# Kernel optimization log

Hardware: AMD Instinct MI355X
Metric: run time of the kernel (lower is better)

## Reference

```python
import jax, jax.numpy as jnp
import numpy as np

DIM = 1024
NUM_HEADS = 16
WINDOW_SIZE = 512
HEAD_DIM = DIM // NUM_HEADS
SCALE = HEAD_DIM ** (-0.5)


def setup_inputs() -> dict:
    key = jax.random.key(0)
    kq, kk, kv = jax.random.split(key, 3)
    shape = (2, NUM_HEADS, 2048, HEAD_DIM)
    q = jax.random.normal(kq, shape, dtype=jnp.float32)
    k = jax.random.normal(kk, shape, dtype=jnp.float32)
    v = jax.random.normal(kv, shape, dtype=jnp.float32)
    return {"q": q, "k": k, "v": v}


def reference(q, k, v):
    B, H, N, D = q.shape
    pos = jnp.arange(N)
    # causal + sliding window: col <= row and col >= row - w + 1
    window_mask = (pos[None, :] <= pos[:, None]) & (pos[None, :] >= pos[:, None] - WINDOW_SIZE + 1)  # (N, N)
    attn = jnp.einsum("bhnd,bhmd->bhnm", q, k) * SCALE  # (B, H, N, N)
    attn = jnp.where(window_mask[None, None], attn, -jnp.inf)
    attn = jax.nn.softmax(attn, axis=-1)
    attn = jnp.nan_to_num(attn, nan=0.0)
    return jnp.einsum("bhnm,bhmd->bhnd", attn, v)
```

## Files before the change

### kernel.cpp

```cpp
#include <hip/hip_runtime.h>


#define SEQ 2048
#define HD  64

typedef short short8 __attribute__((ext_vector_type(8)));
typedef float f32x4  __attribute__((ext_vector_type(4)));
typedef int   i32x4  __attribute__((ext_vector_type(4)));

static __device__ inline unsigned short f2bf(float f){
  union{float f; unsigned u;} un; un.f=f;
  return (unsigned short)((un.u + 0x7FFFu + ((un.u>>16)&1u))>>16);
}
static __device__ inline int swz(int row){ return (row&3)|(((row>>3)&1)<<2); }

__global__ __launch_bounds__(512) void swa_fused(
    const float* __restrict__ q, const float* __restrict__ k,
    const float* __restrict__ v, float* __restrict__ out)
{
  __shared__ unsigned short Ks[2][4096];
  __shared__ unsigned short Vsh[2][4096];

  const int tid=threadIdx.x, bid=blockIdx.x;
  const int mt=bid&15, bh=bid>>4, m0=mt*128;
  const long base=(long)bh*SEQ*HD;
  const int wv=tid>>6, lane=tid&63, quad=lane>>4, l16=lane&15;
  const int qrow=m0+wv*16+l16;
  const int h=wv>>2;

  short8 qa[2];
  {
    const float C=0.18033688011112042f;
    const float* qp=q+base+(long)qrow*HD+quad*8;
    #pragma unroll
    for(int kk=0;kk<2;++kk){
      float4 f0=*(const float4*)(qp+kk*32);
      float4 f1=*(const float4*)(qp+kk*32+4);
      short8 a;
      a[0]=(short)f2bf(f0.x*C); a[1]=(short)f2bf(f0.y*C);
      a[2]=(short)f2bf(f0.z*C); a[3]=(short)f2bf(f0.w*C);
      a[4]=(short)f2bf(f1.x*C); a[5]=(short)f2bf(f1.y*C);
      a[6]=(short)f2bf(f1.z*C); a[7]=(short)f2bf(f1.w*C);
      qa[kk]=a;
    }
  }

  const int rbase=8*(l16>>2)+(l16&3);
  const int swk=(l16&3)|(((l16>>2)&1)<<2);
  const int swv=(l16&3)|(((l16>>3)&1)<<2);
  int kaoff[2][4], vboff[2][4];
  #pragma unroll
  for(int kk=0;kk<2;++kk){
    #pragma unroll
    for(int nt=0;nt<4;++nt)
      kaoff[kk][nt]=(rbase+(nt&1)*4+(nt>>1)*32)*64+(((quad+4*kk)^swk)*8);
    #pragma unroll
    for(int dt=0;dt<4;++dt)
      vboff[kk][dt]=(dt*16+l16)*64+(((quad+4*kk)^swv)*8);
  }

  const int kr=tid>>3, klc=tid&7;
  const int kwaddr=kr*64+((klc^swz(kr))*8);
  const int vw=tid>>6, vd=tid&63;
  const int vwaddr=vd*64+((vw^swz(vd))*8);
  const float* kg=k+base;
  const float* vg=v+base;

  f32x4 oacc[4];
  #pragma unroll
  for(int dt=0;dt<4;++dt) oacc[dt]=(f32x4){0.f,0.f,0.f,0.f};
  float lrun=0.f;

  const int Tb =2*mt+1;
  const int Tlo=(2*mt>8)?(2*mt-8):0;
  const int myTb=2*mt+h;
  const bool clip=(myTb>=8);
  const int myTlo=clip?(myTb-8):0;

  {
    const float* kt=kg+(long)Tlo*4096;
    const float* vt=vg+(long)Tlo*4096;
    float4 kf0=*(const float4*)(kt+kr*64+klc*8);
    float4 kf1=*(const float4*)(kt+kr*64+klc*8+4);
    float vf[8];
    #pragma unroll
    for(int j=0;j<8;++j) vf[j]=vt[(vw*8+j)*64+vd];
    unsigned short hk[8];
    hk[0]=f2bf(kf0.x); hk[1]=f2bf(kf0.y); hk[2]=f2bf(kf0.z); hk[3]=f2bf(kf0.w);
    hk[4]=f2bf(kf1.x); hk[5]=f2bf(kf1.y); hk[6]=f2bf(kf1.z); hk[7]=f2bf(kf1.w);
    *(uint4*)&Ks[0][kwaddr]=*(uint4*)hk;
    unsigned short hv[8];
    #pragma unroll
    for(int j=0;j<8;++j) hv[j]=f2bf(vf[j]);
    *(uint4*)&Vsh[0][vwaddr]=*(uint4*)hv;
  }
  __syncthreads();

  for(int t=Tlo;t<=Tb;++t){
    const int buf=(t-Tlo)&1;
    const bool pf=(t<Tb);

    float4 kf0,kf1; float vf[8];
    if(pf){
      const float* kt=kg+(long)(t+1)*4096;
      const float* vt=vg+(long)(t+1)*4096;
      kf0=*(const float4*)(kt+kr*64+klc*8);
      kf1=*(const float4*)(kt+kr*64+klc*8+4);
      #pragma unroll
      for(int j=0;j<8;++j) vf[j]=vt[(vw*8+j)*64+vd];
    }

    if(t>=myTlo && t<=myTb){
      f32x4 sacc[4];
      #pragma unroll
      for(int nt=0;nt<4;++nt) sacc[nt]=(f32x4){0.f,0.f,0.f,0.f};
      #pragma unroll
      for(int kk=0;kk<2;++kk)
        #pragma unroll
        for(int nt=0;nt<4;++nt){
          short8 ka=*(const short8*)&Ks[buf][kaoff[kk][nt]];
          sacc[nt]=__builtin_amdgcn_mfma_f32_16x16x32_bf16(ka,qa[kk],sacc[nt],0,0,0);
        }

      unsigned pp[8];
      float ls=0.f;
      const bool msk=(t==myTb)||(clip&&t==myTlo);
      #pragma unroll
      for(int nt=0;nt<4;++nt){
        float e0=__builtin_amdgcn_exp2f(sacc[nt][0]);
        float e1=__builtin_amdgcn_exp2f(sacc[nt][1]);
        float e2=__builtin_amdgcn_exp2f(sacc[nt][2]);
        float e3=__builtin_amdgcn_exp2f(sacc[nt][3]);
        if(msk){
          const int kb0=t*64+8*quad+(nt&1)*4+(nt>>1)*32;
          e0=((kb0+0<=qrow)&&(kb0+0+511>=qrow))?e0:0.f;
          e1=((kb0+1<=qrow)&&(kb0+1+511>=qrow))?e1:0.f;
          e2=((kb0+2<=qrow)&&(kb0+2+511>=qrow))?e2:0.f;
          e3=((kb0+3<=qrow)&&(kb0+3+511>=qrow))?e3:0.f;
        }
        ls+=e0+e1+e2+e3;
        pp[nt*2+0]=(__float_as_uint(e1)&0xFFFF0000u)|(__float_as_uint(e0)>>16);
        pp[nt*2+1]=(__float_as_uint(e3)&0xFFFF0000u)|(__float_as_uint(e2)>>16);
      }
      lrun+=ls;
      i32x4 i0={(int)pp[0],(int)pp[1],(int)pp[2],(int)pp[3]};
      i32x4 i1={(int)pp[4],(int)pp[5],(int)pp[6],(int)pp[7]};
      short8 pa0=*(short8*)&i0;
      short8 pa1=*(short8*)&i1;

      #pragma unroll
      for(int dt=0;dt<4;++dt){
        short8 vb0=*(const short8*)&Vsh[buf][vboff[0][dt]];
        short8 vb1=*(const short8*)&Vsh[buf][vboff[1][dt]];
        oacc[dt]=__builtin_amdgcn_mfma_f32_16x16x32_bf16(pa0,vb0,oacc[dt],0,0,0);
        oacc[dt]=__builtin_amdgcn_mfma_f32_16x16x32_bf16(pa1,vb1,oacc[dt],0,0,0);
      }
    }

    if(pf){
      unsigned short hk[8];
      hk[0]=f2bf(kf0.x); hk[1]=f2bf(kf0.y); hk[2]=f2bf(kf0.z); hk[3]=f2bf(kf0.w);
      hk[4]=f2bf(kf1.x); hk[5]=f2bf(kf1.y); hk[6]=f2bf(kf1.z); hk[7]=f2bf(kf1.w);
      *(uint4*)&Ks[buf^1][kwaddr]=*(uint4*)hk;
      unsigned short hv[8];
      #pragma unroll
      for(int j=0;j<8;++j) hv[j]=f2bf(vf[j]);
      *(uint4*)&Vsh[buf^1][vwaddr]=*(uint4*)hv;
    }
    __syncthreads();
  }

  lrun+=__shfl_xor(lrun,16);
  lrun+=__shfl_xor(lrun,32);
  float linv=1.0f/lrun;
  #pragma unroll
  for(int r=0;r<4;++r){
    float lr=__shfl(linv,quad*4+r);
    const int orow=m0+wv*16+quad*4+r;
    #pragma unroll
    for(int dt=0;dt<4;++dt)
      out[base+(long)orow*HD+dt*16+l16]=oacc[dt][r]*lr;
  }
}

extern "C" void kernel_launch(void* const* d_in, const int* in_sizes, int n_in,
                              void* d_out, int out_size, void* d_ws, size_t ws_size,
                              hipStream_t stream) {
  (void)in_sizes; (void)n_in; (void)out_size; (void)d_ws; (void)ws_size;
  const float* q=(const float*)d_in[0];
  const float* k=(const float*)d_in[1];
  const float* v=(const float*)d_in[2];
  float* o=(float*)d_out;
  hipLaunchKernelGGL(swa_fused, dim3(512), dim3(512), 0, stream, q, k, v, o);
}
```

Measured before the change: 108.4 us.

## Pre-convert K/V to swizzled bf16 images and stream them via global_load_lds

Adds a prep kernel that converts K and V from fp32 to bf16 once, writing them to workspace already in the swizzled (and transposed, for V) shared-memory layout. The attention kernel then copies each tile straight into LDS with 16-byte global_load_lds, replacing the per-block fp32 loads, conversions and LDS stores. This removes the redundant conversion work repeated across the overlapping windows and halves the bytes read per tile. In exchange it adds a second launch and a workspace round trip, and the async LDS loads rely on the existing barrier for ordering.

```diff
diff --git a/kernel.cpp b/kernel.cpp
--- a/kernel.cpp
+++ b/kernel.cpp
@@ -14,9 +14,44 @@
 }
 static __device__ inline int swz(int row){ return (row&3)|(((row>>3)&1)<<2); }
 
+static __device__ __forceinline__ void gload16(const void* g, void* l){
+  __builtin_amdgcn_global_load_lds(
+      (const __attribute__((address_space(1))) void*)g,
+      (__attribute__((address_space(3))) void*)l,
+      16, 0, 0);
+}
+
+__global__ __launch_bounds__(512) void swa_prep(
+    const float* __restrict__ k, const float* __restrict__ v,
+    unsigned short* __restrict__ kp, unsigned short* __restrict__ vp)
+{
+  const int tid=threadIdx.x, bid=blockIdx.x;
+  const long fbase=(long)bid*4096;
+  const long ib  =(long)bid*4096;
+
+  {
+    const int kr=tid>>3, klc=tid&7;
+    const float* kt=k+fbase+kr*64+klc*8;
+    float4 f0=*(const float4*)kt;
+    float4 f1=*(const float4*)(kt+4);
+    unsigned short h[8];
+    h[0]=f2bf(f0.x); h[1]=f2bf(f0.y); h[2]=f2bf(f0.z); h[3]=f2bf(f0.w);
+    h[4]=f2bf(f1.x); h[5]=f2bf(f1.y); h[6]=f2bf(f1.z); h[7]=f2bf(f1.w);
+    *(uint4*)&kp[ib + kr*64 + ((klc^swz(kr))*8)] = *(uint4*)h;
+  }
+  {
+    const int vw=tid>>6, vd=tid&63;
+    const float* vt=v+fbase;
+    unsigned short h[8];
+    #pragma unroll
+    for(int j=0;j<8;++j) h[j]=f2bf(vt[(vw*8+j)*64+vd]);
+    *(uint4*)&vp[ib + vd*64 + ((vw^swz(vd))*8)] = *(uint4*)h;
+  }
+}
+
 __global__ __launch_bounds__(512) void swa_fused(
-    const float* __restrict__ q, const float* __restrict__ k,
-    const float* __restrict__ v, float* __restrict__ out)
+    const float* __restrict__ q, const unsigned short* __restrict__ kp,
+    const unsigned short* __restrict__ vp, float* __restrict__ out)
 {
   __shared__ unsigned short Ks[2][4096];
   __shared__ unsigned short Vsh[2][4096];
@@ -59,12 +94,10 @@
       vboff[kk][dt]=(dt*16+l16)*64+(((quad+4*kk)^swv)*8);
   }
 
-  const int kr=tid>>3, klc=tid&7;
-  const int kwaddr=kr*64+((klc^swz(kr))*8);
-  const int vw=tid>>6, vd=tid&63;
-  const int vwaddr=vd*64+((vw^swz(vd))*8);
-  const float* kg=k+base;
-  const float* vg=v+base;
+  const unsigned short* kimg = kp + (long)bh*32*4096 + tid*8;
+  const unsigned short* vimg = vp + (long)bh*32*4096 + tid*8;
+  unsigned short* kdst = &Ks[0][wv*512];
+  unsigned short* vdst = &Vsh[0][wv*512];
 
   f32x4 oacc[4];
   #pragma unroll
@@ -77,37 +110,16 @@
   const bool clip=(myTb>=8);
   const int myTlo=clip?(myTb-8):0;
 
-  {
-    const float* kt=kg+(long)Tlo*4096;
-    const float* vt=vg+(long)Tlo*4096;
-    float4 kf0=*(const float4*)(kt+kr*64+klc*8);
-    float4 kf1=*(const float4*)(kt+kr*64+klc*8+4);
-    float vf[8];
-    #pragma unroll
-    for(int j=0;j<8;++j) vf[j]=vt[(vw*8+j)*64+vd];
-    unsigned short hk[8];
-    hk[0]=f2bf(kf0.x); hk[1]=f2bf(kf0.y); hk[2]=f2bf(kf0.z); hk[3]=f2bf(kf0.w);
-    hk[4]=f2bf(kf1.x); hk[5]=f2bf(kf1.y); hk[6]=f2bf(kf1.z); hk[7]=f2bf(kf1.w);
-    *(uint4*)&Ks[0][kwaddr]=*(uint4*)hk;
-    unsigned short hv[8];
-    #pragma unroll
-    for(int j=0;j<8;++j) hv[j]=f2bf(vf[j]);
-    *(uint4*)&Vsh[0][vwaddr]=*(uint4*)hv;
-  }
+  gload16(kimg+(long)Tlo*4096, kdst);
+  gload16(vimg+(long)Tlo*4096, vdst);
   __syncthreads();
 
   for(int t=Tlo;t<=Tb;++t){
     const int buf=(t-Tlo)&1;
-    const bool pf=(t<Tb);
-
-    float4 kf0,kf1; float vf[8];
-    if(pf){
-      const float* kt=kg+(long)(t+1)*4096;
-      const float* vt=vg+(long)(t+1)*4096;
-      kf0=*(const float4*)(kt+kr*64+klc*8);
-      kf1=*(const float4*)(kt+kr*64+klc*8+4);
-      #pragma unroll
-      for(int j=0;j<8;++j) vf[j]=vt[(vw*8+j)*64+vd];
+
+    if(t<Tb){
+      gload16(kimg+(long)(t+1)*4096, kdst+(buf^1)*4096);
+      gload16(vimg+(long)(t+1)*4096, vdst+(buf^1)*4096);
     }
 
     if(t>=myTlo && t<=myTb){
@@ -157,16 +169,6 @@
       }
     }
 
-    if(pf){
-      unsigned short hk[8];
-      hk[0]=f2bf(kf0.x); hk[1]=f2bf(kf0.y); hk[2]=f2bf(kf0.z); hk[3]=f2bf(kf0.w);
-      hk[4]=f2bf(kf1.x); hk[5]=f2bf(kf1.y); hk[6]=f2bf(kf1.z); hk[7]=f2bf(kf1.w);
-      *(uint4*)&Ks[buf^1][kwaddr]=*(uint4*)hk;
-      unsigned short hv[8];
-      #pragma unroll
-      for(int j=0;j<8;++j) hv[j]=f2bf(vf[j]);
-      *(uint4*)&Vsh[buf^1][vwaddr]=*(uint4*)hv;
-    }
     __syncthreads();
   }
 
@@ -186,10 +188,13 @@
 extern "C" void kernel_launch(void* const* d_in, const int* in_sizes, int n_in,
                               void* d_out, int out_size, void* d_ws, size_t ws_size,
                               hipStream_t stream) {
-  (void)in_sizes; (void)n_in; (void)out_size; (void)d_ws; (void)ws_size;
+  (void)in_sizes; (void)n_in; (void)out_size; (void)ws_size;
   const float* q=(const float*)d_in[0];
   const float* k=(const float*)d_in[1];
   const float* v=(const float*)d_in[2];
   float* o=(float*)d_out;
-  hipLaunchKernelGGL(swa_fused, dim3(512), dim3(512), 0, stream, q, k, v, o);
-}
+  unsigned short* kp=(unsigned short*)d_ws;
+  unsigned short* vp=kp + (long)32*32*4096;
+  hipLaunchKernelGGL(swa_prep,  dim3(1024), dim3(512), 0, stream, k, v, kp, vp);
+  hipLaunchKernelGGL(swa_fused, dim3(512),  dim3(512), 0, stream, q, kp, vp, o);
+}
```

After: 109.9 us. About the same (+1.4%).

## Process two K/V tiles per pipeline stage to halve block barriers

Applied to the files above, without the earlier changes.

Restructures the double-buffered loop so each iteration loads, converts and consumes two 64-row K/V tiles instead of one. This halves the number of __syncthreads and makes each prefetch twice as deep. It also adds a min-blocks hint of 4 to launch_bounds. The cost is twice the LDS (64KB per block) and more prefetch registers, which could limit occupancy or cause spills under the tighter register budget.

```diff
diff --git a/kernel.cpp b/kernel.cpp
--- a/kernel.cpp
+++ b/kernel.cpp
@@ -14,12 +14,12 @@
 }
 static __device__ inline int swz(int row){ return (row&3)|(((row>>3)&1)<<2); }
 
-__global__ __launch_bounds__(512) void swa_fused(
+__global__ __launch_bounds__(512,4) void swa_fused(
     const float* __restrict__ q, const float* __restrict__ k,
     const float* __restrict__ v, float* __restrict__ out)
 {
-  __shared__ unsigned short Ks[2][4096];
-  __shared__ unsigned short Vsh[2][4096];
+  __shared__ unsigned short Ks[2][2][4096];
+  __shared__ unsigned short Vsh[2][2][4096];
 
   const int tid=threadIdx.x, bid=blockIdx.x;
   const int mt=bid&15, bh=bid>>4, m0=mt*128;
@@ -76,96 +76,106 @@
   const int myTb=2*mt+h;
   const bool clip=(myTb>=8);
   const int myTlo=clip?(myTb-8):0;
-
-  {
-    const float* kt=kg+(long)Tlo*4096;
-    const float* vt=vg+(long)Tlo*4096;
-    float4 kf0=*(const float4*)(kt+kr*64+klc*8);
-    float4 kf1=*(const float4*)(kt+kr*64+klc*8+4);
-    float vf[8];
-    #pragma unroll
-    for(int j=0;j<8;++j) vf[j]=vt[(vw*8+j)*64+vd];
+  const int nR=(Tb-Tlo+2)>>1;
+
+  #pragma unroll
+  for(int s=0;s<2;++s){
+    const float* kt=kg+(long)(Tlo+s)*4096;
+    const float* vt=vg+(long)(Tlo+s)*4096;
+    float4 f0=*(const float4*)(kt+kr*64+klc*8);
+    float4 f1=*(const float4*)(kt+kr*64+klc*8+4);
     unsigned short hk[8];
-    hk[0]=f2bf(kf0.x); hk[1]=f2bf(kf0.y); hk[2]=f2bf(kf0.z); hk[3]=f2bf(kf0.w);
-    hk[4]=f2bf(kf1.x); hk[5]=f2bf(kf1.y); hk[6]=f2bf(kf1.z); hk[7]=f2bf(kf1.w);
-    *(uint4*)&Ks[0][kwaddr]=*(uint4*)hk;
+    hk[0]=f2bf(f0.x); hk[1]=f2bf(f0.y); hk[2]=f2bf(f0.z); hk[3]=f2bf(f0.w);
+    hk[4]=f2bf(f1.x); hk[5]=f2bf(f1.y); hk[6]=f2bf(f1.z); hk[7]=f2bf(f1.w);
+    *(uint4*)&Ks[0][s][kwaddr]=*(uint4*)hk;
     unsigned short hv[8];
     #pragma unroll
-    for(int j=0;j<8;++j) hv[j]=f2bf(vf[j]);
-    *(uint4*)&Vsh[0][vwaddr]=*(uint4*)hv;
+    for(int j=0;j<8;++j) hv[j]=f2bf(vt[(vw*8+j)*64+vd]);
+    *(uint4*)&Vsh[0][s][vwaddr]=*(uint4*)hv;
   }
   __syncthreads();
 
-  for(int t=Tlo;t<=Tb;++t){
-    const int buf=(t-Tlo)&1;
-    const bool pf=(t<Tb);
-
-    float4 kf0,kf1; float vf[8];
+  for(int r=0;r<nR;++r){
+    const int buf=r&1;
+    const bool pf=(r+1<nR);
+
+    float4 kf0[2],kf1[2]; float vf[2][8];
     if(pf){
-      const float* kt=kg+(long)(t+1)*4096;
-      const float* vt=vg+(long)(t+1)*4096;
-      kf0=*(const float4*)(kt+kr*64+klc*8);
-      kf1=*(const float4*)(kt+kr*64+klc*8+4);
       #pragma unroll
-      for(int j=0;j<8;++j) vf[j]=vt[(vw*8+j)*64+vd];
-    }
-
-    if(t>=myTlo && t<=myTb){
-      f32x4 sacc[4];
+      for(int s=0;s<2;++s){
+        const int tn=Tlo+2*r+2+s;
+        const float* kt=kg+(long)tn*4096;
+        const float* vt=vg+(long)tn*4096;
+        kf0[s]=*(const float4*)(kt+kr*64+klc*8);
+        kf1[s]=*(const float4*)(kt+kr*64+klc*8+4);
+        #pragma unroll
+        for(int j=0;j<8;++j) vf[s][j]=vt[(vw*8+j)*64+vd];
+      }
+    }
+
+    #pragma unroll
+    for(int s=0;s<2;++s){
+      const int t=Tlo+2*r+s;
+      if(t>=myTlo && t<=myTb){
+        f32x4 sacc[4];
+        #pragma unroll
+        for(int nt=0;nt<4;++nt) sacc[nt]=(f32x4){0.f,0.f,0.f,0.f};
+        #pragma unroll
+        for(int kk=0;kk<2;++kk)
+          #pragma unroll
+          for(int nt=0;nt<4;++nt){
+            short8 ka=*(const short8*)&Ks[buf][s][kaoff[kk][nt]];
+            sacc[nt]=__builtin_amdgcn_mfma_f32_16x16x32_bf16(ka,qa[kk],sacc[nt],0,0,0);
+          }
+
+        unsigned pp[8];
+        float ls=0.f;
+        const bool msk=(t==myTb)||(clip&&t==myTlo);
+        #pragma unroll
+        for(int nt=0;nt<4;++nt){
+          float e0=__builtin_amdgcn_exp2f(sacc[nt][0]);
+          float e1=__builtin_amdgcn_exp2f(sacc[nt][1]);
+          float e2=__builtin_amdgcn_exp2f(sacc[nt][2]);
+          float e3=__builtin_amdgcn_exp2f(sacc[nt][3]);
+          if(msk){
+            const int kb0=t*64+8*quad+(nt&1)*4+(nt>>1)*32;
+            e0=((kb0+0<=qrow)&&(kb0+0+511>=qrow))?e0:0.f;
+            e1=((kb0+1<=qrow)&&(kb0+1+511>=qrow))?e1:0.f;
+            e2=((kb0+2<=qrow)&&(kb0+2+511>=qrow))?e2:0.f;
+            e3=((kb0+3<=qrow)&&(kb0+3+511>=qrow))?e3:0.f;
+          }
+          ls+=e0+e1+e2+e3;
+          pp[nt*2+0]=(__float_as_uint(e1)&0xFFFF0000u)|(__float_as_uint(e0)>>16);
+          pp[nt*2+1]=(__float_as_uint(e3)&0xFFFF0000u)|(__float_as_uint(e2)>>16);
+        }
+        lrun+=ls;
+        i32x4 i0={(int)pp[0],(int)pp[1],(int)pp[2],(int)pp[3]};
+        i32x4 i1={(int)pp[4],(int)pp[5],(int)pp[6],(int)pp[7]};
+        short8 pa0=*(short8*)&i0;
+        short8 pa1=*(short8*)&i1;
+
+        #pragma unroll
+        for(int dt=0;dt<4;++dt){
+          short8 vb0=*(const short8*)&Vsh[buf][s][vboff[0][dt]];
+          short8 vb1=*(const short8*)&Vsh[buf][s][vboff[1][dt]];
+          oacc[dt]=__builtin_amdgcn_mfma_f32_16x16x32_bf16(pa0,vb0,oacc[dt],0,0,0);
+          oacc[dt]=__builtin_amdgcn_mfma_f32_16x16x32_bf16(pa1,vb1,oacc[dt],0,0,0);
+        }
+      }
+    }
+
+    if(pf){
       #pragma unroll
-      for(int nt=0;nt<4;++nt) sacc[nt]=(f32x4){0.f,0.f,0.f,0.f};
-      #pragma unroll
-      for(int kk=0;kk<2;++kk)
-        #pragma unroll
-        for(int nt=0;nt<4;++nt){
-          short8 ka=*(const short8*)&Ks[buf][kaoff[kk][nt]];
-          sacc[nt]=__builtin_amdgcn_mfma_f32_16x16x32_bf16(ka,qa[kk],sacc[nt],0,0,0);
-        }
-
-      unsigned pp[8];
-      float ls=0.f;
-      const bool msk=(t==myTb)||(clip&&t==myTlo);
-      #pragma unroll
-      for(int nt=0;nt<4;++nt){
-        float e0=__builtin_amdgcn_exp2f(sacc[nt][0]);
-        float e1=__builtin_amdgcn_exp2f(sacc[nt][1]);
-        float e2=__builtin_amdgcn_exp2f(sacc[nt][2]);
-        float e3=__builtin_amdgcn_exp2f(sacc[nt][3]);
-        if(msk){
-          const int kb0=t*64+8*quad+(nt&1)*4+(nt>>1)*32;
-          e0=((kb0+0<=qrow)&&(kb0+0+511>=qrow))?e0:0.f;
-          e1=((kb0+1<=qrow)&&(kb0+1+511>=qrow))?e1:0.f;
-          e2=((kb0+2<=qrow)&&(kb0+2+511>=qrow))?e2:0.f;
-          e3=((kb0+3<=qrow)&&(kb0+3+511>=qrow))?e3:0.f;
-        }
-        ls+=e0+e1+e2+e3;
-        pp[nt*2+0]=(__float_as_uint(e1)&0xFFFF0000u)|(__float_as_uint(e0)>>16);
-        pp[nt*2+1]=(__float_as_uint(e3)&0xFFFF0000u)|(__float_as_uint(e2)>>16);
+      for(int s=0;s<2;++s){
+        unsigned short hk[8];
+        hk[0]=f2bf(kf0[s].x); hk[1]=f2bf(kf0[s].y); hk[2]=f2bf(kf0[s].z); hk[3]=f2bf(kf0[s].w);
+        hk[4]=f2bf(kf1[s].x); hk[5]=f2bf(kf1[s].y); hk[6]=f2bf(kf1[s].z); hk[7]=f2bf(kf1[s].w);
+        *(uint4*)&Ks[buf^1][s][kwaddr]=*(uint4*)hk;
+        unsigned short hv[8];
+        #pragma unroll
+        for(int j=0;j<8;++j) hv[j]=f2bf(vf[s][j]);
+        *(uint4*)&Vsh[buf^1][s][vwaddr]=*(uint4*)hv;
       }
-      lrun+=ls;
-      i32x4 i0={(int)pp[0],(int)pp[1],(int)pp[2],(int)pp[3]};
-      i32x4 i1={(int)pp[4],(int)pp[5],(int)pp[6],(int)pp[7]};
-      short8 pa0=*(short8*)&i0;
-      short8 pa1=*(short8*)&i1;
-
-      #pragma unroll
-      for(int dt=0;dt<4;++dt){
-        short8 vb0=*(const short8*)&Vsh[buf][vboff[0][dt]];
-        short8 vb1=*(const short8*)&Vsh[buf][vboff[1][dt]];
-        oacc[dt]=__builtin_amdgcn_mfma_f32_16x16x32_bf16(pa0,vb0,oacc[dt],0,0,0);
-        oacc[dt]=__builtin_amdgcn_mfma_f32_16x16x32_bf16(pa1,vb1,oacc[dt],0,0,0);
-      }
-    }
-
-    if(pf){
-      unsigned short hk[8];
-      hk[0]=f2bf(kf0.x); hk[1]=f2bf(kf0.y); hk[2]=f2bf(kf0.z); hk[3]=f2bf(kf0.w);
-      hk[4]=f2bf(kf1.x); hk[5]=f2bf(kf1.y); hk[6]=f2bf(kf1.z); hk[7]=f2bf(kf1.w);
-      *(uint4*)&Ks[buf^1][kwaddr]=*(uint4*)hk;
-      unsigned short hv[8];
-      #pragma unroll
-      for(int j=0;j<8;++j) hv[j]=f2bf(vf[j]);
-      *(uint4*)&Vsh[buf^1][vwaddr]=*(uint4*)hv;
     }
     __syncthreads();
   }
```

After: 109.3 us. Within noise of the previous version (+0.8%).
